# Kernel tuning notes

Hardware: AMD Instinct MI355X
Metric: run time of the kernel (lower is better)

The kernel has to match this reference:

```python
import jax, jax.numpy as jnp
import numpy as np
from jax import lax

DN = ('NCHW', 'OIHW', 'NCHW')
NUM_IN_CAPS = 1152  # 32 * 6 * 6
NUM_OUT_CAPS = 10
IN_CAP_DIM = 8
OUT_CAP_DIM = 16
ROUTING_ITERS = 3


def squash(x):
    # unit_v * |x|^2 / (1 + |x|^2), norm over last dim
    n = jnp.linalg.norm(x, axis=-1, keepdims=True)
    return (x / n) * (n * n / (1.0 + n * n))


def setup_inputs() -> dict:
    key = jax.random.key(0)
    ks = jax.random.split(key, 12)
    B = 256
    return {
        'x': jax.random.normal(ks[0], (B, 1, 28, 28), jnp.float32),
        'conv1_w': jax.random.normal(ks[1], (256, 1, 9, 9), jnp.float32) * 0.05,
        'conv1_b': jnp.zeros((256,), jnp.float32),
        'pconv_w': jax.random.normal(ks[2], (256, 256, 9, 9), jnp.float32) * 0.02,
        'pconv_b': jnp.zeros((256,), jnp.float32),
        'W_caps': jax.random.normal(ks[3], (NUM_IN_CAPS, NUM_OUT_CAPS, OUT_CAP_DIM, IN_CAP_DIM), jnp.float32),
        'dec_w1': jax.random.normal(ks[4], (160, 512), jnp.float32) * 0.05,
        'dec_b1': jnp.zeros((512,), jnp.float32),
        'dec_w2': jax.random.normal(ks[5], (512, 1024), jnp.float32) * 0.04,
        'dec_b2': jnp.zeros((1024,), jnp.float32),
        'dec_w3': jax.random.normal(ks[6], (1024, 784), jnp.float32) * 0.03,
        'dec_b3': jnp.zeros((784,), jnp.float32),
    }


def reference(x, conv1_w, conv1_b, pconv_w, pconv_b, W_caps,
              dec_w1, dec_b1, dec_w2, dec_b2, dec_w3, dec_b3):
    # conv1: 1 -> 256, k9, s1, no activation (faithful to source)
    h = lax.conv_general_dilated(x, conv1_w, (1, 1), 'VALID', dimension_numbers=DN)
    h = h + conv1_b[None, :, None, None]  # (B,256,20,20)
    # primary caps conv: 256 -> 32*8, k9, s2
    h = lax.conv_general_dilated(h, pconv_w, (2, 2), 'VALID', dimension_numbers=DN)
    h = h + pconv_b[None, :, None, None]  # (B,256,6,6)
    B = h.shape[0]
    u_in = squash(h.reshape(B, -1, IN_CAP_DIM))  # (B,1152,8)
    # prediction vectors u_hat: (B,1152,10,16)
    u = jnp.einsum('ijab,nib->nija', W_caps, u_in)
    # routing-by-agreement; b is shared across batch and accumulates batch-summed agreement (faithful)
    b = jnp.zeros((NUM_IN_CAPS, NUM_OUT_CAPS), u.dtype)
    v = None
    for r in range(ROUTING_ITERS + 1):
        c = jax.nn.softmax(b, axis=-1)             # (1152,10)
        s = jnp.einsum('ij,nija->nja', c, u)        # (B,10,16)
        v = squash(s)
        if r < ROUTING_ITERS:
            b = b + jnp.einsum('nija,nja->ij', u, v)
    # decoder path: mask by predicted class
    logits = jnp.linalg.norm(v, axis=-1)            # (B,10)
    label = jnp.argmax(logits, axis=1)
    one_hot = jax.nn.one_hot(label, NUM_OUT_CAPS, dtype=v.dtype)
    recon = (one_hot[..., None] * v).reshape(B, NUM_OUT_CAPS * OUT_CAP_DIM)
    recon = jax.nn.relu(recon @ dec_w1 + dec_b1)
    recon = jax.nn.relu(recon @ dec_w2 + dec_b2)
    recon = jax.nn.sigmoid(recon @ dec_w3 + dec_b3)  # (B,784)
    return (v, recon)
```

## Files before the change

kernel.cpp:

```cpp
#include <hip/hip_runtime.h>
#include <hip/hip_fp16.h>
#include <math.h>


typedef __attribute__((ext_vector_type(8))) _Float16 half8;
typedef __attribute__((ext_vector_type(8))) short short8;
typedef __attribute__((ext_vector_type(4))) float floatx4;

__device__ __forceinline__ unsigned short f16bits(float v) {
    _Float16 h = (_Float16)v;
    unsigned short b;
    __builtin_memcpy(&b, &h, 2);
    return b;
}
__device__ __forceinline__ float f16back(unsigned short b) {
    _Float16 h;
    __builtin_memcpy(&h, &b, 2);
    return (float)h;
}
__device__ __forceinline__ void load_lds16(const void* g, void* l) {
    __builtin_amdgcn_global_load_lds(
        (const __attribute__((address_space(1))) unsigned int*)g,
        (__attribute__((address_space(3))) unsigned int*)l, 16, 0, 0);
}

__global__ __launch_bounds__(256, 2) void conv1_kernel(
    const float* __restrict__ x, const float* __restrict__ w,
    const float* __restrict__ bias, unsigned short* __restrict__ xpack)
{
    __shared__ float xs[784];
    __shared__ float wl[64 * 81];
    int t = threadIdx.x;
    int n = blockIdx.x;
    int cot = blockIdx.y;

    for (int j = t; j < 784; j += 256) xs[j] = x[n * 784 + j];
    {
        int co_s = t >> 2, k0 = (t & 3) * 21;
        const float* wsrc = w + (size_t)(cot * 64 + co_s) * 81;
        #pragma unroll
        for (int k = 0; k < 21; ++k)
            if (k0 + k < 81) wl[co_s * 81 + k0 + k] = wsrc[k0 + k];
    }
    __syncthreads();

    int co_l = t & 63, slot = t >> 6;
    int co = cot * 64 + co_l;
    float bv = bias[co];
    for (int r5 = 0; r5 < 5; ++r5) {
        int py = slot * 5 + r5;
        float acc[20];
        #pragma unroll
        for (int i = 0; i < 20; i++) acc[i] = bv;
        #pragma unroll
        for (int ky = 0; ky < 9; ++ky) {
            float xr[28];
            const float4* rowp = (const float4*)&xs[(py + ky) * 28];
            #pragma unroll
            for (int q = 0; q < 7; q++) {
                float4 v4 = rowp[q];
                xr[4*q] = v4.x; xr[4*q+1] = v4.y; xr[4*q+2] = v4.z; xr[4*q+3] = v4.w;
            }
            #pragma unroll
            for (int kx = 0; kx < 9; ++kx) {
                float wv = wl[co_l * 81 + ky * 9 + kx];
                #pragma unroll
                for (int px = 0; px < 20; ++px) acc[px] += wv * xr[px + kx];
            }
        }
        #pragma unroll
        for (int px = 0; px < 20; ++px) {
            float v = acc[px];
            unsigned short h = f16bits(v);
            unsigned short l = f16bits(v - f16back(h));
            size_t pix = (size_t)n * 400 + py * 20 + px;
            xpack[pix * 512 + co] = h;
            xpack[pix * 512 + 256 + co] = l;
        }
    }
}

__global__ __launch_bounds__(256) void wpack_kernel(
    const float* __restrict__ w, unsigned short* __restrict__ wp)
{
    int tid = blockIdx.x * 256 + threadIdx.x;
    if (tid >= 648 * 16 * 64) return;
    int lane = tid & 63, g = (tid >> 6) & 15, gs = tid >> 10;
    int cb = gs & 7, kk = gs >> 3;
    int ky = kk / 9, kx = kk - ky * 9;
    int n16 = lane & 15, q = lane >> 4;
    int co = g * 16 + n16;
    unsigned short hv[8];
    #pragma unroll
    for (int j = 0; j < 8; ++j) {
        int ci = cb * 32 + q * 8 + j;
        hv[j] = f16bits(w[((size_t)co * 256 + ci) * 81 + ky * 9 + kx]);
    }
    unsigned short* dst = wp + ((size_t)gs * 16 + g) * 512 + lane * 8;
    *(short8*)dst = *(short8*)hv;
}

__global__ __launch_bounds__(256, 3) void pconv_mfma_kernel(
    const unsigned short* __restrict__ xp, const unsigned short* __restrict__ wp,
    __half* __restrict__ P6)
{
    __shared__ unsigned char lds[49152];
    int t = threadIdx.x;
    int lane = t & 63;
    int w = __builtin_amdgcn_readfirstlane(t >> 6);
    int mtile = blockIdx.x, kc = blockIdx.y;
    int m16 = lane & 15, q = lane >> 4;

    unsigned int asrc[2];
    #pragma unroll
    for (int j = 0; j < 2; ++j) {
        int r = w * 16 + j * 8 + (lane >> 3);
        if (r > 47) r = 47;
        int m = mtile * 48 + r;
        int n = m / 36, pos = m - n * 36;
        int oy = pos / 6, ox = pos - oy * 6;
        int pixbase = n * 400 + oy * 40 + ox * 2;
        int pp = (lane & 7) ^ (lane >> 3);
        int partoff = (pp < 4) ? pp * 16 : 512 + (pp - 4) * 16;
        asrc[j] = (unsigned int)(pixbase * 1024 + partoff);
    }
    const char* xb = (const char*)xp;
    const char* wb = (const char*)wp;

    floatx4 acc[3][4];
    #pragma unroll
    for (int a = 0; a < 3; ++a)
        #pragma unroll
        for (int b = 0; b < 4; ++b) acc[a][b] = (floatx4){0.f, 0.f, 0.f, 0.f};

    int slot_hi = (q ^ (m16 & 7)) * 16;
    int slot_lo = slot_hi ^ 64;

    auto stageP = [&](int p, int buf) {
        if (w < 3) {
            #pragma unroll
            for (int e = 0; e < 2; ++e) {
                int s = 2 * p + e; if (s > 161) s = 161;
                int gs = kc * 162 + s;
                int kk = gs >> 3, cb = gs & 7;
                int ky = kk / 9, kx = kk - ky * 9;
                unsigned int delta = (unsigned int)((ky * 20 + kx) * 1024 + cb * 64);
                #pragma unroll
                for (int j = 0; j < 2; ++j)
                    load_lds16(xb + asrc[j] + delta,
                               (void*)(lds + buf * 12288 + e * 6144 + w * 2048 + j * 1024));
            }
        }
    };
    auto loadB = [&](int s, half8* B) {
        if (s > 161) s = 161;
        int gs = kc * 162 + s;
        #pragma unroll
        for (int c = 0; c < 4; ++c)
            B[c] = *(const half8*)(wb + ((size_t)gs * 16 + (w * 4 + c)) * 1024 + lane * 16);
    };
    auto compute = [&](int buf, int e, half8* B) {
        #pragma unroll
        for (int ms = 0; ms < 3; ++ms) {
            const char* base = (const char*)lds + buf * 12288 + e * 6144 + (ms * 16 + m16) * 128;
            half8 Ah = *(const half8*)(base + slot_hi);
            half8 Al = *(const half8*)(base + slot_lo);
            #pragma unroll
            for (int c = 0; c < 4; ++c) {
                acc[ms][c] = __builtin_amdgcn_mfma_f32_16x16x32_f16(Ah, B[c], acc[ms][c], 0, 0, 0);
                acc[ms][c] = __builtin_amdgcn_mfma_f32_16x16x32_f16(Al, B[c], acc[ms][c], 0, 0, 0);
            }
        }
    };

    half8 Ba0[4], Ba1[4], Bb0[4], Bb1[4];

    stageP(0, 0);
    stageP(1, 1);
    loadB(0, Ba0); loadB(1, Ba1);
    asm volatile("s_waitcnt vmcnt(12)" ::: "memory");
    __builtin_amdgcn_s_barrier();

#define PSTEP(PI, BUF, NBUF, C0, C1, N0, N1)                    \
    stageP((PI) + 2, NBUF);                                     \
    loadB(2 * (PI) + 2, N0); loadB(2 * (PI) + 3, N1);           \
    compute(BUF, 0, C0); compute(BUF, 1, C1);                   \
    asm volatile("s_waitcnt vmcnt(12)" ::: "memory");           \
    __builtin_amdgcn_s_barrier();

    for (int p = 0; p < 78; p += 6) {
        PSTEP(p + 0, 0, 2, Ba0, Ba1, Bb0, Bb1)
        PSTEP(p + 1, 1, 0, Bb0, Bb1, Ba0, Ba1)
        PSTEP(p + 2, 2, 1, Ba0, Ba1, Bb0, Bb1)
        PSTEP(p + 3, 0, 2, Bb0, Bb1, Ba0, Ba1)
        PSTEP(p + 4, 1, 0, Ba0, Ba1, Bb0, Bb1)
        PSTEP(p + 5, 2, 1, Bb0, Bb1, Ba0, Ba1)
    }
    PSTEP(78, 0, 2, Ba0, Ba1, Bb0, Bb1)
    PSTEP(79, 1, 0, Bb0, Bb1, Ba0, Ba1)
    PSTEP(80, 2, 1, Ba0, Ba1, Bb0, Bb1)
#undef PSTEP

    __half* outp = P6 + ((size_t)kc * 9216 + (size_t)mtile * 48) * 256;
    #pragma unroll
    for (int ms = 0; ms < 3; ++ms)
        #pragma unroll
        for (int r = 0; r < 4; ++r) {
            int ml = ms * 16 + q * 4 + r;
            #pragma unroll
            for (int c = 0; c < 4; ++c) {
                int co = w * 64 + c * 16 + m16;
                outp[ml * 256 + co] = __float2half(acc[ms][c][r]);
            }
        }
}

__global__ __launch_bounds__(256) void squash_u_kernel(
    const __half* __restrict__ P6, const float* __restrict__ pb, float* __restrict__ u)
{
    int cap = blockIdx.x * 256 + threadIdx.x;
    int n = cap / 1152;
    int capl = cap - n * 1152;
    float z[8]; float n2 = 0.f;
    #pragma unroll
    for (int b = 0; b < 8; ++b) {
        int q2 = capl * 8 + b;
        int co = q2 / 36;
        int pos = q2 - co * 36;
        int m = n * 36 + pos;
        float s = 0.f;
        #pragma unroll
        for (int kc = 0; kc < 4; ++kc)
            s += __half2float(P6[((size_t)kc * 9216 + m) * 256 + co]);
        s += pb[co];
        z[b] = s; n2 += s * s;
    }
    float sc = sqrtf(n2) / (1.0f + n2);
    float4* op = (float4*)(u + (size_t)cap * 8);
    op[0] = make_float4(z[0]*sc, z[1]*sc, z[2]*sc, z[3]*sc);
    op[1] = make_float4(z[4]*sc, z[5]*sc, z[6]*sc, z[7]*sc);
}

__global__ __launch_bounds__(256, 2) void s_kernel(
    const float* __restrict__ b, const float* __restrict__ u,
    const float* __restrict__ W, float* __restrict__ sbuf)
{
    __shared__ float cs[24][10];
    int t = threadIdx.x;
    int a = t & 15, nl = t >> 4;
    int nt = blockIdx.x;
    int bz = blockIdx.y;
    int i0 = bz * 24;
    int n0 = nt * 32 + nl * 2;

    if (t < 24) {
        int i = i0 + t;
        float e[10], m = -1e30f;
        #pragma unroll
        for (int j = 0; j < 10; j++) { e[j] = b[i * 10 + j]; m = fmaxf(m, e[j]); }
        float sum = 0.f;
        #pragma unroll
        for (int j = 0; j < 10; j++) { e[j] = expf(e[j] - m); sum += e[j]; }
        float inv = 1.f / sum;
        #pragma unroll
        for (int j = 0; j < 10; j++) cs[t][j] = e[j] * inv;
    }
    __syncthreads();

    float acc[2][10];
    #pragma unroll
    for (int r = 0; r < 2; ++r)
        #pragma unroll
        for (int j = 0; j < 10; ++j) acc[r][j] = 0.f;

    for (int i = i0; i < i0 + 24; ++i) {
        float4 u0[2], u1[2];
        #pragma unroll
        for (int r = 0; r < 2; ++r) {
            const float4* up = (const float4*)&u[(size_t)(n0 + r) * 9216 + (size_t)i * 8];
            u0[r] = up[0]; u1[r] = up[1];
        }
        #pragma unroll
        for (int j = 0; j < 10; ++j) {
            const float4* wpt = (const float4*)&W[(((size_t)i * 10 + j) * 16 + a) * 8];
            float4 w0 = wpt[0], w1 = wpt[1];
            float cij = cs[i - i0][j];
            #pragma unroll
            for (int r = 0; r < 2; ++r) {
                float d = w0.x*u0[r].x + w0.y*u0[r].y + w0.z*u0[r].z + w0.w*u0[r].w
                        + w1.x*u1[r].x + w1.y*u1[r].y + w1.z*u1[r].z + w1.w*u1[r].w;
                acc[r][j] += cij * d;
            }
        }
    }
    #pragma unroll
    for (int r = 0; r < 2; ++r)
        #pragma unroll
        for (int j = 0; j < 10; ++j)
            sbuf[(size_t)bz * 40960 + (((size_t)(n0 + r) * 10 + j) * 16) + a] = acc[r][j];
}

__global__ __launch_bounds__(256) void squash_v_kernel(const float* __restrict__ sbuf,
                                float* __restrict__ v, float* __restrict__ vout)
{
    int t = threadIdx.x;
    int a = t & 15;
    int idx = blockIdx.x * 16 + (t >> 4);
    float s = 0.f;
    #pragma unroll
    for (int z = 0; z < 48; ++z) s += sbuf[(size_t)z * 40960 + idx * 16 + a];
    float n2 = s * s;
    n2 += __shfl_xor(n2, 1);
    n2 += __shfl_xor(n2, 2);
    n2 += __shfl_xor(n2, 4);
    n2 += __shfl_xor(n2, 8);
    float sc = sqrtf(n2) / (1.0f + n2);
    float y = s * sc;
    v[idx * 16 + a] = y;
    if (vout) vout[idx * 16 + a] = y;
}

__global__ __launch_bounds__(192) void bupd_kernel(
    const float* __restrict__ u, const float* __restrict__ v,
    const float* __restrict__ W, float* __restrict__ b)
{
    int i0 = blockIdx.x * 4;
    int n0 = blockIdx.y * 128;
    int t = threadIdx.x;
    if (t >= 160) return;
    int j = t >> 4, a = t & 15;
    float g4[4][8];
    #pragma unroll
    for (int g = 0; g < 4; ++g)
        #pragma unroll
        for (int k = 0; k < 8; ++k) g4[g][k] = 0.f;

    for (int n = n0; n < n0 + 128; ++n) {
        float vv = v[n * 160 + t];
        const float4* ub = (const float4*)&u[(size_t)n * 9216 + (size_t)i0 * 8];
        #pragma unroll
        for (int g = 0; g < 4; ++g) {
            float4 q0 = ub[g * 2], q1 = ub[g * 2 + 1];
            g4[g][0] += q0.x * vv; g4[g][1] += q0.y * vv; g4[g][2] += q0.z * vv; g4[g][3] += q0.w * vv;
            g4[g][4] += q1.x * vv; g4[g][5] += q1.y * vv; g4[g][6] += q1.z * vv; g4[g][7] += q1.w * vv;
        }
    }
    #pragma unroll
    for (int g = 0; g < 4; ++g) {
        int i = i0 + g;
        const float4* wpt = (const float4*)&W[(((size_t)i * 10 + j) * 16 + a) * 8];
        float4 w0 = wpt[0], w1 = wpt[1];
        float p = w0.x*g4[g][0] + w0.y*g4[g][1] + w0.z*g4[g][2] + w0.w*g4[g][3]
                + w1.x*g4[g][4] + w1.y*g4[g][5] + w1.z*g4[g][6] + w1.w*g4[g][7];
        p += __shfl_xor(p, 1);
        p += __shfl_xor(p, 2);
        p += __shfl_xor(p, 4);
        p += __shfl_xor(p, 8);
        if (a == 0) atomicAdd(&b[i * 10 + j], p);
    }
}

__global__ __launch_bounds__(256) void mask_kernel(const float* __restrict__ v, float* __restrict__ out)
{
    int t = threadIdx.x;
    int a = t & 15, nl = t >> 4;
    int n = blockIdx.x * 16 + nl;
    const float* vp = &v[n * 160];
    int best = 0; float bestn2 = -1.f;
    #pragma unroll
    for (int j = 0; j < 10; ++j) {
        float y = vp[j * 16 + a];
        float n2 = y * y;
        n2 += __shfl_xor(n2, 1);
        n2 += __shfl_xor(n2, 2);
        n2 += __shfl_xor(n2, 4);
        n2 += __shfl_xor(n2, 8);
        if (n2 > bestn2) { bestn2 = n2; best = j; }
    }
    #pragma unroll
    for (int j = 0; j < 10; ++j)
        out[n * 160 + j * 16 + a] = (j == best) ? vp[j * 16 + a] : 0.f;
}

template<int K, int KCH, int O>
__global__ __launch_bounds__(256, 2) void mlp_part_kernel(
    const float* __restrict__ X, const float* __restrict__ Wm,
    float* __restrict__ partial)
{
    __shared__ float XS[KCH * 16];
    int t = threadIdx.x;
    int og = t & 63, ns = t >> 6;
    int n0 = blockIdx.x * 16;
    int o = blockIdx.y * 256 + og * 4;
    int o_c = min(o, O - 4);
    int ks = blockIdx.z;
    int kc0 = ks * KCH;

    for (int idx = t; idx < KCH * 16; idx += 256) {
        int k_l = idx >> 4, n_l = idx & 15;
        XS[k_l * 16 + n_l] = X[(size_t)(n0 + n_l) * K + kc0 + k_l];
    }
    __syncthreads();

    float acc[4][4];
    #pragma unroll
    for (int r = 0; r < 4; ++r)
        #pragma unroll
        for (int q = 0; q < 4; ++q) acc[r][q] = 0.f;

    #pragma unroll 8
    for (int k = 0; k < KCH; ++k) {
        float4 wv = *(const float4*)&Wm[(size_t)(kc0 + k) * O + o_c];
        float4 xs4 = *(const float4*)&XS[k * 16 + ns * 4];
        acc[0][0] += xs4.x * wv.x; acc[0][1] += xs4.x * wv.y; acc[0][2] += xs4.x * wv.z; acc[0][3] += xs4.x * wv.w;
        acc[1][0] += xs4.y * wv.x; acc[1][1] += xs4.y * wv.y; acc[1][2] += xs4.y * wv.z; acc[1][3] += xs4.y * wv.w;
        acc[2][0] += xs4.z * wv.x; acc[2][1] += xs4.z * wv.y; acc[2][2] += xs4.z * wv.z; acc[2][3] += xs4.z * wv.w;
        acc[3][0] += xs4.w * wv.x; acc[3][1] += xs4.w * wv.y; acc[3][2] += xs4.w * wv.z; acc[3][3] += xs4.w * wv.w;
    }

    if (o < O) {
        float* pp = partial + ((size_t)ks * 256 + n0 + ns * 4) * O + o;
        #pragma unroll
        for (int r = 0; r < 4; ++r)
            *(float4*)(pp + (size_t)r * O) = make_float4(acc[r][0], acc[r][1], acc[r][2], acc[r][3]);
    }
}

template<int KS, int O, int ACT>
__global__ __launch_bounds__(256) void mlp_reduce_kernel(
    const float* __restrict__ partial, const float* __restrict__ bias,
    float* __restrict__ out)
{
    int n = blockIdx.y;
    int o = (blockIdx.x * 256 + threadIdx.x) * 4;
    if (o >= O) return;
    float4 s = make_float4(0.f, 0.f, 0.f, 0.f);
    #pragma unroll
    for (int ks = 0; ks < KS; ++ks) {
        float4 p = *(const float4*)&partial[((size_t)ks * 256 + n) * O + o];
        s.x += p.x; s.y += p.y; s.z += p.z; s.w += p.w;
    }
    float4 bv = *(const float4*)&bias[o];
    float r[4] = {s.x + bv.x, s.y + bv.y, s.z + bv.z, s.w + bv.w};
    #pragma unroll
    for (int q = 0; q < 4; ++q)
        r[q] = (ACT == 0) ? fmaxf(r[q], 0.f) : (1.f / (1.f + expf(-r[q])));
    *(float4*)&out[(size_t)n * O + o] = make_float4(r[0], r[1], r[2], r[3]);
}

extern "C" void kernel_launch(void* const* d_in, const int* in_sizes, int n_in,
                              void* d_out, int out_size, void* d_ws, size_t ws_size,
                              hipStream_t stream)
{
    const float* x       = (const float*)d_in[0];
    const float* conv1_w = (const float*)d_in[1];
    const float* conv1_b = (const float*)d_in[2];
    const float* pconv_w = (const float*)d_in[3];
    const float* pconv_b = (const float*)d_in[4];
    const float* W_caps  = (const float*)d_in[5];
    const float* dec_w1  = (const float*)d_in[6];
    const float* dec_b1  = (const float*)d_in[7];
    const float* dec_w2  = (const float*)d_in[8];
    const float* dec_b2  = (const float*)d_in[9];
    const float* dec_w3  = (const float*)d_in[10];
    const float* dec_b3  = (const float*)d_in[11];
    float* out = (float*)d_out;

    float* ws = (float*)d_ws;
    size_t off = 0;
    auto alloc = [&](size_t nf) { float* p = ws + off; off += (nf + 63) & ~(size_t)63; return p; };
    unsigned short* xpack = (unsigned short*)alloc(26214400);
    unsigned short* wpack = (unsigned short*)alloc(2654208);
    __half* P6  = (__half*)alloc(4718592);
    float* u_in = alloc(2359296);
    float* bbuf = alloc(11520);
    float* sbuf = alloc(48 * 40960);
    float* vbuf = alloc(40960);
    float* rin  = alloc(40960);
    float* mpart = alloc(8 * 256 * 1024);
    float* h1   = alloc(131072);
    float* h2   = alloc(262144);

    hipMemsetAsync(bbuf, 0, 11520 * sizeof(float), stream);

    wpack_kernel<<<(648 * 16 * 64 + 255) / 256, 256, 0, stream>>>(pconv_w, wpack);
    conv1_kernel<<<dim3(256, 4), 256, 0, stream>>>(x, conv1_w, conv1_b, xpack);
    pconv_mfma_kernel<<<dim3(192, 4), 256, 0, stream>>>(xpack, wpack, P6);
    squash_u_kernel<<<1152, 256, 0, stream>>>(P6, pconv_b, u_in);

    for (int r = 0; r < 4; ++r) {
        s_kernel<<<dim3(8, 48), 256, 0, stream>>>(bbuf, u_in, W_caps, sbuf);
        squash_v_kernel<<<160, 256, 0, stream>>>(sbuf, vbuf, (r == 3) ? out : nullptr);
        if (r < 3) bupd_kernel<<<dim3(288, 2), 192, 0, stream>>>(u_in, vbuf, W_caps, bbuf);
    }

    mask_kernel<<<16, 256, 0, stream>>>(vbuf, rin);

    mlp_part_kernel<160, 80, 512><<<dim3(16, 2, 2), 256, 0, stream>>>(rin, dec_w1, mpart);
    mlp_reduce_kernel<2, 512, 0><<<dim3(1, 256), 256, 0, stream>>>(mpart, dec_b1, h1);
    mlp_part_kernel<512, 128, 1024><<<dim3(16, 4, 4), 256, 0, stream>>>(h1, dec_w2, mpart);
    mlp_reduce_kernel<4, 1024, 0><<<dim3(1, 256), 256, 0, stream>>>(mpart, dec_b2, h2);
    mlp_part_kernel<1024, 128, 784><<<dim3(16, 4, 8), 256, 0, stream>>>(h2, dec_w3, mpart);
    mlp_reduce_kernel<8, 784, 1><<<dim3(1, 256), 256, 0, stream>>>(mpart, dec_b3, out + 40960);
}
```

Measured before the change: 710.5 us.

## Fuse routing squash, mask and MLP reductions via last-block atomic counters

The per-slab sbuf of partial s sums is replaced by atomicAdd into a single accumulator. The last block to finish, found with a global counter, squashes v, zeroes the accumulator, and on the final iteration also applies the class mask. The MLP reduce kernels are likewise folded into the partial-GEMM kernels with per-tile counters. This removes eight kernel launches and the 48-way partial buffer traffic, at the cost of float atomics, which make summation order nondeterministic, and a serialized single-block tail for the squash and mask work.

```diff
diff --git a/kernel.cpp b/kernel.cpp
--- a/kernel.cpp
+++ b/kernel.cpp
@@ -241,11 +241,14 @@
     op[1] = make_float4(z[4]*sc, z[5]*sc, z[6]*sc, z[7]*sc);
 }
 
-__global__ __launch_bounds__(256, 2) void s_kernel(
+__global__ __launch_bounds__(256, 2) void route_s_kernel(
     const float* __restrict__ b, const float* __restrict__ u,
-    const float* __restrict__ W, float* __restrict__ sbuf)
+    const float* __restrict__ W, float* __restrict__ svacc,
+    float* __restrict__ v, unsigned int* __restrict__ cnt,
+    float* __restrict__ vout, float* __restrict__ rin)
 {
     __shared__ float cs[24][10];
+    __shared__ int lastf;
     int t = threadIdx.x;
     int a = t & 15, nl = t >> 4;
     int nt = blockIdx.x;
@@ -297,27 +300,63 @@
     for (int r = 0; r < 2; ++r)
         #pragma unroll
         for (int j = 0; j < 10; ++j)
-            sbuf[(size_t)bz * 40960 + (((size_t)(n0 + r) * 10 + j) * 16) + a] = acc[r][j];
-}
-
-__global__ __launch_bounds__(256) void squash_v_kernel(const float* __restrict__ sbuf,
-                                float* __restrict__ v, float* __restrict__ vout)
-{
-    int t = threadIdx.x;
-    int a = t & 15;
-    int idx = blockIdx.x * 16 + (t >> 4);
-    float s = 0.f;
-    #pragma unroll
-    for (int z = 0; z < 48; ++z) s += sbuf[(size_t)z * 40960 + idx * 16 + a];
-    float n2 = s * s;
-    n2 += __shfl_xor(n2, 1);
-    n2 += __shfl_xor(n2, 2);
-    n2 += __shfl_xor(n2, 4);
-    n2 += __shfl_xor(n2, 8);
-    float sc = sqrtf(n2) / (1.0f + n2);
-    float y = s * sc;
-    v[idx * 16 + a] = y;
-    if (vout) vout[idx * 16 + a] = y;
+            atomicAdd(&svacc[(((size_t)(n0 + r) * 10 + j) * 16) + a], acc[r][j]);
+
+    __threadfence();
+    if (t == 0) lastf = (atomicAdd(cnt, 1u) == 8u * 48u - 1u) ? 1 : 0;
+    __syncthreads();
+    if (!lastf) return;
+    __threadfence();
+
+    for (int pr = t; pr < 2560; pr += 256) {
+        float4* sp = (float4*)&svacc[(size_t)pr * 16];
+        float4 x0 = sp[0], x1 = sp[1], x2 = sp[2], x3 = sp[3];
+        float n2 = x0.x*x0.x + x0.y*x0.y + x0.z*x0.z + x0.w*x0.w
+                 + x1.x*x1.x + x1.y*x1.y + x1.z*x1.z + x1.w*x1.w
+                 + x2.x*x2.x + x2.y*x2.y + x2.z*x2.z + x2.w*x2.w
+                 + x3.x*x3.x + x3.y*x3.y + x3.z*x3.z + x3.w*x3.w;
+        float sc = sqrtf(n2) / (1.0f + n2);
+        float4 y0 = make_float4(x0.x*sc, x0.y*sc, x0.z*sc, x0.w*sc);
+        float4 y1 = make_float4(x1.x*sc, x1.y*sc, x1.z*sc, x1.w*sc);
+        float4 y2 = make_float4(x2.x*sc, x2.y*sc, x2.z*sc, x2.w*sc);
+        float4 y3 = make_float4(x3.x*sc, x3.y*sc, x3.z*sc, x3.w*sc);
+        float4* vp = (float4*)&v[(size_t)pr * 16];
+        vp[0] = y0; vp[1] = y1; vp[2] = y2; vp[3] = y3;
+        if (vout) {
+            float4* op = (float4*)&vout[(size_t)pr * 16];
+            op[0] = y0; op[1] = y1; op[2] = y2; op[3] = y3;
+        }
+        float4 z4 = make_float4(0.f, 0.f, 0.f, 0.f);
+        sp[0] = z4; sp[1] = z4; sp[2] = z4; sp[3] = z4;
+    }
+    if (t == 0) atomicExch(cnt, 0u);
+
+    if (rin) {
+        __syncthreads();
+        const float* vp = &v[(size_t)t * 160];
+        int best = 0; float bestn2 = -1.f;
+        #pragma unroll
+        for (int j = 0; j < 10; ++j) {
+            const float4* q4 = (const float4*)&vp[j * 16];
+            float4 a0 = q4[0], a1 = q4[1], a2 = q4[2], a3 = q4[3];
+            float n2 = a0.x*a0.x + a0.y*a0.y + a0.z*a0.z + a0.w*a0.w
+                     + a1.x*a1.x + a1.y*a1.y + a1.z*a1.z + a1.w*a1.w
+                     + a2.x*a2.x + a2.y*a2.y + a2.z*a2.z + a2.w*a2.w
+                     + a3.x*a3.x + a3.y*a3.y + a3.z*a3.z + a3.w*a3.w;
+            if (n2 > bestn2) { bestn2 = n2; best = j; }
+        }
+        float* rp = &rin[(size_t)t * 160];
+        #pragma unroll
+        for (int j = 0; j < 10; ++j) {
+            const float4* q4 = (const float4*)&vp[j * 16];
+            float4* o4 = (float4*)&rp[j * 16];
+            if (j == best) { o4[0] = q4[0]; o4[1] = q4[1]; o4[2] = q4[2]; o4[3] = q4[3]; }
+            else {
+                float4 z4 = make_float4(0.f, 0.f, 0.f, 0.f);
+                o4[0] = z4; o4[1] = z4; o4[2] = z4; o4[3] = z4;
+            }
+        }
+    }
 }
 
 __global__ __launch_bounds__(192) void bupd_kernel(
@@ -360,34 +399,15 @@
     }
 }
 
-__global__ __launch_bounds__(256) void mask_kernel(const float* __restrict__ v, float* __restrict__ out)
-{
-    int t = threadIdx.x;
-    int a = t & 15, nl = t >> 4;
-    int n = blockIdx.x * 16 + nl;
-    const float* vp = &v[n * 160];
-    int best = 0; float bestn2 = -1.f;
-    #pragma unroll
-    for (int j = 0; j < 10; ++j) {
-        float y = vp[j * 16 + a];
-        float n2 = y * y;
-        n2 += __shfl_xor(n2, 1);
-        n2 += __shfl_xor(n2, 2);
-        n2 += __shfl_xor(n2, 4);
-        n2 += __shfl_xor(n2, 8);
-        if (n2 > bestn2) { bestn2 = n2; best = j; }
-    }
-    #pragma unroll
-    for (int j = 0; j < 10; ++j)
-        out[n * 160 + j * 16 + a] = (j == best) ? vp[j * 16 + a] : 0.f;
-}
-
-template<int K, int KCH, int O>
-__global__ __launch_bounds__(256, 2) void mlp_part_kernel(
+template<int K, int KCH, int O, int ACT>
+__global__ __launch_bounds__(256, 2) void mlp_fused_kernel(
     const float* __restrict__ X, const float* __restrict__ Wm,
-    float* __restrict__ partial)
+    const float* __restrict__ bias, float* __restrict__ partial,
+    float* __restrict__ out, unsigned int* __restrict__ cnts)
 {
     __shared__ float XS[KCH * 16];
+    __shared__ int lastf;
+    const int KS = K / KCH;
     int t = threadIdx.x;
     int og = t & 63, ns = t >> 6;
     int n0 = blockIdx.x * 16;
@@ -424,28 +444,32 @@
         for (int r = 0; r < 4; ++r)
             *(float4*)(pp + (size_t)r * O) = make_float4(acc[r][0], acc[r][1], acc[r][2], acc[r][3]);
     }
-}
-
-template<int KS, int O, int ACT>
-__global__ __launch_bounds__(256) void mlp_reduce_kernel(
-    const float* __restrict__ partial, const float* __restrict__ bias,
-    float* __restrict__ out)
-{
-    int n = blockIdx.y;
-    int o = (blockIdx.x * 256 + threadIdx.x) * 4;
-    if (o >= O) return;
-    float4 s = make_float4(0.f, 0.f, 0.f, 0.f);
-    #pragma unroll
-    for (int ks = 0; ks < KS; ++ks) {
-        float4 p = *(const float4*)&partial[((size_t)ks * 256 + n) * O + o];
-        s.x += p.x; s.y += p.y; s.z += p.z; s.w += p.w;
-    }
-    float4 bv = *(const float4*)&bias[o];
-    float r[4] = {s.x + bv.x, s.y + bv.y, s.z + bv.z, s.w + bv.w};
-    #pragma unroll
-    for (int q = 0; q < 4; ++q)
-        r[q] = (ACT == 0) ? fmaxf(r[q], 0.f) : (1.f / (1.f + expf(-r[q])));
-    *(float4*)&out[(size_t)n * O + o] = make_float4(r[0], r[1], r[2], r[3]);
+
+    __threadfence();
+    int ci = blockIdx.y * gridDim.x + blockIdx.x;
+    if (t == 0) lastf = (atomicAdd(&cnts[ci], 1u) == (unsigned)(KS - 1)) ? 1 : 0;
+    __syncthreads();
+    if (!lastf) return;
+    __threadfence();
+
+    if (o < O) {
+        float4 bv = *(const float4*)&bias[o];
+        #pragma unroll
+        for (int r = 0; r < 4; ++r) {
+            int n = n0 + ns * 4 + r;
+            float4 s = make_float4(0.f, 0.f, 0.f, 0.f);
+            for (int z = 0; z < KS; ++z) {
+                float4 p = *(const float4*)&partial[((size_t)z * 256 + n) * O + o];
+                s.x += p.x; s.y += p.y; s.z += p.z; s.w += p.w;
+            }
+            float rr[4] = {s.x + bv.x, s.y + bv.y, s.z + bv.z, s.w + bv.w};
+            #pragma unroll
+            for (int q = 0; q < 4; ++q)
+                rr[q] = (ACT == 0) ? fmaxf(rr[q], 0.f) : (1.f / (1.f + expf(-rr[q])));
+            *(float4*)&out[(size_t)n * O + o] = make_float4(rr[0], rr[1], rr[2], rr[3]);
+        }
+    }
+    if (t == 0) atomicExch(&cnts[ci], 0u);
 }
 
 extern "C" void kernel_launch(void* const* d_in, const int* in_sizes, int n_in,
@@ -474,14 +498,15 @@
     __half* P6  = (__half*)alloc(4718592);
     float* u_in = alloc(2359296);
     float* bbuf = alloc(11520);
-    float* sbuf = alloc(48 * 40960);
+    float* svacc = alloc(40960);
+    unsigned int* cnts = (unsigned int*)alloc(256);
     float* vbuf = alloc(40960);
     float* rin  = alloc(40960);
     float* mpart = alloc(8 * 256 * 1024);
     float* h1   = alloc(131072);
     float* h2   = alloc(262144);
 
-    hipMemsetAsync(bbuf, 0, 11520 * sizeof(float), stream);
+    hipMemsetAsync(bbuf, 0, (11520 + 40960 + 256) * sizeof(float), stream);
 
     wpack_kernel<<<(648 * 16 * 64 + 255) / 256, 256, 0, stream>>>(pconv_w, wpack);
     conv1_kernel<<<dim3(256, 4), 256, 0, stream>>>(x, conv1_w, conv1_b, xpack);
@@ -489,17 +514,13 @@
     squash_u_kernel<<<1152, 256, 0, stream>>>(P6, pconv_b, u_in);
 
     for (int r = 0; r < 4; ++r) {
-        s_kernel<<<dim3(8, 48), 256, 0, stream>>>(bbuf, u_in, W_caps, sbuf);
-        squash_v_kernel<<<160, 256, 0, stream>>>(sbuf, vbuf, (r == 3) ? out : nullptr);
+        route_s_kernel<<<dim3(8, 48), 256, 0, stream>>>(
+            bbuf, u_in, W_caps, svacc, vbuf, &cnts[64],
+            (r == 3) ? out : nullptr, (r == 3) ? rin : nullptr);
         if (r < 3) bupd_kernel<<<dim3(288, 2), 192, 0, stream>>>(u_in, vbuf, W_caps, bbuf);
     }
 
-    mask_kernel<<<16, 256, 0, stream>>>(vbuf, rin);
-
-    mlp_part_kernel<160, 80, 512><<<dim3(16, 2, 2), 256, 0, stream>>>(rin, dec_w1, mpart);
-    mlp_reduce_kernel<2, 512, 0><<<dim3(1, 256), 256, 0, stream>>>(mpart, dec_b1, h1);
-    mlp_part_kernel<512, 128, 1024><<<dim3(16, 4, 4), 256, 0, stream>>>(h1, dec_w2, mpart);
-    mlp_reduce_kernel<4, 1024, 0><<<dim3(1, 256), 256, 0, stream>>>(mpart, dec_b2, h2);
-    mlp_part_kernel<1024, 128, 784><<<dim3(16, 4, 8), 256, 0, stream>>>(h2, dec_w3, mpart);
-    mlp_reduce_kernel<8, 784, 1><<<dim3(1, 256), 256, 0, stream>>>(mpart, dec_b3, out + 40960);
-}
+    mlp_fused_kernel<160, 80, 512, 0><<<dim3(16, 2, 2), 256, 0, stream>>>(rin, dec_w1, dec_b1, mpart, h1, cnts);
+    mlp_fused_kernel<512, 128, 1024, 0><<<dim3(16, 4, 4), 256, 0, stream>>>(h1, dec_w2, dec_b2, mpart, h2, cnts);
+    mlp_fused_kernel<1024, 128, 784, 1><<<dim3(16, 4, 8), 256, 0, stream>>>(h2, dec_w3, dec_b3, mpart, out + 40960, cnts);
+}
```

Result: slower. 962.0 us (+35.4%).
